# Performance work log

Hardware: AMD Instinct MI355X
Metric: run time of the kernel (lower is better)

The kernel has to match this reference:

```python
import jax, jax.numpy as jnp
import numpy as np

N = 100000
E = 1600000
IN_C = 256
OUT_C = 64


def setup_inputs() -> dict:
    key = jax.random.key(0)
    k1, k2, k3, k4, k5 = jax.random.split(key, 5)
    x = jax.random.normal(k1, (N, IN_C), dtype=jnp.float32)
    edge_index = jax.random.randint(k2, (2, E), 0, N, dtype=jnp.int64)
    edge_weight = jax.random.uniform(k3, (E,), dtype=jnp.float32)
    # GCNConv linear weight (Glorot-style scale) and bias
    W = jax.random.normal(k4, (IN_C, OUT_C), dtype=jnp.float32) * (1.0 / np.sqrt(IN_C))
    b = jax.random.normal(k5, (OUT_C,), dtype=jnp.float32) * 0.01
    return {"x": x, "edge_index": edge_index, "edge_weight": edge_weight, "W": W, "b": b}


def reference(x, edge_index, edge_weight, W, b):
    n = x.shape[0]
    row, col = edge_index[0], edge_index[1]  # source -> target (PyG source_to_target flow)
    # add self-loops with weight 1.0 (GCNConv default add_self_loops=True)
    loop = jnp.arange(n, dtype=edge_index.dtype)
    row = jnp.concatenate([row, loop])
    col = jnp.concatenate([col, loop])
    ew = jnp.concatenate([edge_weight, jnp.ones((n,), dtype=x.dtype)])
    # symmetric normalization: deg computed on target nodes
    deg = jax.ops.segment_sum(ew, col, num_segments=n)
    dinv = jnp.where(deg > 0, jax.lax.rsqrt(deg), 0.0)
    norm = dinv[row] * ew * dinv[col]  # [E+N]
    # dense linear transform first (fewer FLOPs than transforming per-edge)
    h = x @ W  # [N, OUT_C]
    # gather messages from source, scale, scatter-add to target
    out = jax.ops.segment_sum(norm[:, None] * h[row], col, num_segments=n)
    out = out + b
    # activation is None -> module returns (val, ()); we return val
    return out
```

## Files before the change

kernel.cpp:

```cpp
#include <hip/hip_runtime.h>
#include <hip/hip_fp16.h>


#define BS 256
#define EPB2 4096
#define BSH 8
#define CAP 4608

typedef unsigned long long u64;
typedef unsigned int u32;
typedef unsigned short u16;
typedef unsigned char u8;

typedef __attribute__((ext_vector_type(8))) short bf16x8;
typedef __attribute__((ext_vector_type(4))) float f32x4;

__device__ inline u16 f2bf(float f) {
    u32 u = __float_as_uint(f);
    return (u16)((u + 0x7fffu + ((u >> 16) & 1u)) >> 16);
}
__device__ inline u32 pack2bf(float a, float b) {
    return (u32)f2bf(a) | ((u32)f2bf(b) << 16);
}

#define GBM2 128
#define XAP 40

__global__ __launch_bounds__(BS) void k_g4(const float* __restrict__ x,
                                           const float* __restrict__ W,
                                           u16* __restrict__ hh, int n,
                                           const int* __restrict__ row,
                                           const int* __restrict__ col,
                                           const float* __restrict__ ew,
                                           u32* __restrict__ cursor,
                                           u64* __restrict__ pack,
                                           int nbuck, int nblk2, int e) {
    __shared__ __align__(16) u8 smem[24576];
    const int tid = threadIdx.x;
    const int bi = blockIdx.x;
    const bool isScatter = ((bi % 3) == 2) && (bi / 3 < nblk2);

    if (isScatter) {
        u16* bkt  = (u16*)smem;
        u16* sidx = (u16*)(smem + 8192);
        u32* cnt  = (u32*)(smem + 16384);
        u32* scn  = (u32*)(smem + 18432);
        u32* lpos = (u32*)(smem + 20480);
        u32* gb   = (u32*)(smem + 22528);
        int blk = bi / 3;
        int base = blk * EPB2;
        int ej = e - base; if (ej > EPB2) ej = EPB2;

        cnt[tid] = 0; cnt[tid + 256] = 0;
        __syncthreads();
#pragma unroll
        for (int j = 0; j < 16; ++j) {
            int lj = j * BS + tid;
            if (lj < ej) {
                int b = col[base + lj] >> BSH;
                bkt[lj] = (u16)b;
                atomicAdd(&cnt[b], 1u);
            }
        }
        __syncthreads();
        scn[tid] = cnt[tid];
        scn[tid + 256] = cnt[tid + 256];
        __syncthreads();
        for (int off = 1; off < 512; off <<= 1) {
            u32 a0 = (tid >= off) ? scn[tid - off] : 0u;
            u32 a1 = scn[tid + 256 - off];
            __syncthreads();
            scn[tid] += a0;
            scn[tid + 256] += a1;
            __syncthreads();
        }
        for (int t = tid; t < 512; t += 256) {
            u32 c = cnt[t];
            lpos[t] = scn[t] - c;
            if (c) gb[t] = atomicAdd(&cursor[t], c);
        }
        __syncthreads();
#pragma unroll
        for (int j = 0; j < 16; ++j) {
            int lj = j * BS + tid;
            if (lj < ej) {
                u32 p = atomicAdd(&lpos[bkt[lj]], 1u);
                sidx[p] = (u16)lj;
            }
        }
        __syncthreads();
        for (int p = tid; p < ej; p += 256) {
            int lj = sidx[p];
            int b = bkt[lj];
            int i = base + lj;
            __half eh = __float2half(ew[i]);
            u64 en = (u64)(u32)row[i]
                   | ((u64)(u32)(col[i] & 255) << 32)
                   | ((u64)(u16)__half_as_ushort(eh) << 48);
            u32 local = (u32)p - (scn[b] - cnt[b]) + gb[b];
            if (local < CAP) pack[(size_t)b * CAP + local] = en;
        }
        return;
    }
    int sbefore = bi / 3; if (sbefore > nblk2) sbefore = nblk2;
    const int gid = bi - sbefore;
    u16* xa = (u16*)smem;
    u16* wt = (u16*)(smem + 10240);
    const int lane = tid & 63;
    const int wid  = tid >> 6;
    const int lr = lane & 15;
    const int lg = lane >> 4;
    const int rb = gid * GBM2;
    const int wrow = wid * 32;

    f32x4 acc[2][4];
#pragma unroll
    for (int rt = 0; rt < 2; ++rt)
#pragma unroll
        for (int ct = 0; ct < 4; ++ct) acc[rt][ct] = (f32x4){0.f, 0.f, 0.f, 0.f};

    const int srow = tid >> 1;
    const int skh  = (tid & 1) * 16;
    const int wc   = tid >> 2;
    const int wk   = (tid & 3) * 8;

    for (int kc = 0; kc < 256; kc += 32) {
        {
            int gr = rb + srow; if (gr >= n) gr = n - 1;
            const float4* src = reinterpret_cast<const float4*>(&x[(size_t)gr * 256 + kc + skh]);
            float4 a0 = src[0], a1 = src[1], a2 = src[2], a3 = src[3];
            uint4 v0, v1;
            v0.x = pack2bf(a0.x, a0.y); v0.y = pack2bf(a0.z, a0.w);
            v0.z = pack2bf(a1.x, a1.y); v0.w = pack2bf(a1.z, a1.w);
            v1.x = pack2bf(a2.x, a2.y); v1.y = pack2bf(a2.z, a2.w);
            v1.z = pack2bf(a3.x, a3.y); v1.w = pack2bf(a3.z, a3.w);
            *reinterpret_cast<uint4*>(&xa[srow * XAP + skh]) = v0;
            *reinterpret_cast<uint4*>(&xa[srow * XAP + skh + 8]) = v1;
        }
        {
            float w0 = W[(size_t)(kc + wk + 0) * 64 + wc];
            float w1 = W[(size_t)(kc + wk + 1) * 64 + wc];
            float w2 = W[(size_t)(kc + wk + 2) * 64 + wc];
            float w3 = W[(size_t)(kc + wk + 3) * 64 + wc];
            float w4 = W[(size_t)(kc + wk + 4) * 64 + wc];
            float w5 = W[(size_t)(kc + wk + 5) * 64 + wc];
            float w6 = W[(size_t)(kc + wk + 6) * 64 + wc];
            float w7 = W[(size_t)(kc + wk + 7) * 64 + wc];
            u32* dst = reinterpret_cast<u32*>(&wt[wc * XAP + wk]);
            dst[0] = pack2bf(w0, w1);
            dst[1] = pack2bf(w2, w3);
            dst[2] = pack2bf(w4, w5);
            dst[3] = pack2bf(w6, w7);
        }
        __syncthreads();

        bf16x8 af0 = *reinterpret_cast<const bf16x8*>(&xa[(wrow + lr) * XAP + lg * 8]);
        bf16x8 af1 = *reinterpret_cast<const bf16x8*>(&xa[(wrow + 16 + lr) * XAP + lg * 8]);
#pragma unroll
        for (int ct = 0; ct < 4; ++ct) {
            bf16x8 bfr = *reinterpret_cast<const bf16x8*>(&wt[(ct * 16 + lr) * XAP + lg * 8]);
            acc[0][ct] = __builtin_amdgcn_mfma_f32_16x16x32_bf16(af0, bfr, acc[0][ct], 0, 0, 0);
            acc[1][ct] = __builtin_amdgcn_mfma_f32_16x16x32_bf16(af1, bfr, acc[1][ct], 0, 0, 0);
        }
        __syncthreads();
    }

    u16* eo = (u16*)smem;
#pragma unroll
    for (int rt = 0; rt < 2; ++rt) {
#pragma unroll
        for (int reg = 0; reg < 4; ++reg) {
            int r = wrow + rt * 16 + lg * 4 + reg;
#pragma unroll
            for (int ct = 0; ct < 4; ++ct) {
                eo[r * 64 + ct * 16 + lr] =
                    __half_as_ushort(__float2half(acc[rt][ct][reg]));
            }
        }
    }
    __syncthreads();
    {
        const uint4* src = reinterpret_cast<const uint4*>(eo);
        uint4* dst = reinterpret_cast<uint4*>(hh + (size_t)rb * 64);
#pragma unroll
        for (int i = 0; i < 4; ++i) {
            int idx = i * BS + tid;
            if (rb + (idx >> 3) < n) dst[idx] = src[idx];
        }
    }
}

#define MAXB CAP
__global__ __launch_bounds__(512) void k_b2(const u32* __restrict__ cursor,
                                            u64* __restrict__ pack,
                                            float* __restrict__ dinv,
                                            int* __restrict__ offs,
                                            int* __restrict__ ends,
                                            int n, int nbuck) {
    __shared__ u32 lrow[MAXB];
    __shared__ u16 lew[MAXB];
    __shared__ u8  lcl[MAXB];
    __shared__ u32 cnt[256];
    __shared__ float wdeg[256];
    __shared__ u32 pos[256];
    __shared__ float ldsd[256];
    int b = blockIdx.x;
    int tid = threadIdx.x;
    size_t gbase = (size_t)b * CAP;
    int size = (int)cursor[b];
    if (size > MAXB) size = MAXB;
    if (tid < 256) { cnt[tid] = 0; wdeg[tid] = 0.0f; }
    __syncthreads();
    for (int j = tid; j < size; j += 512) {
        u64 en = pack[gbase + j];
        u32 r = (u32)en;
        u32 cl = (u32)(en >> 32) & 255u;
        u16 eh = (u16)(en >> 48);
        lrow[j] = r;
        lcl[j] = (u8)cl;
        lew[j] = eh;
        atomicAdd(&cnt[cl], 1u);
        atomicAdd(&wdeg[cl], __half2float(__ushort_as_half(eh)));
    }
    __syncthreads();
    u32 myc = (tid < 256) ? cnt[tid] : 0;
    for (int off = 1; off < 256; off <<= 1) {
        u32 t = 0;
        if (tid < 256 && tid >= (u32)off) t = cnt[tid - off];
        __syncthreads();
        if (tid < 256) cnt[tid] += t;
        __syncthreads();
    }
    if (tid < 256) {
        u32 st = cnt[tid] - myc;
        pos[tid] = st;
        float dv = rsqrtf(1.0f + wdeg[tid]);
        ldsd[tid] = dv;
        int c = (b << BSH) + tid;
        if (c < n) {
            dinv[c] = dv;
            offs[c] = (int)(gbase + st);
            ends[c] = (int)(gbase + st + myc);
        }
    }
    __syncthreads();
    for (int j = tid; j < size; j += 512) {
        u32 cl = lcl[j];
        u32 r = atomicAdd(&pos[cl], 1u);
        float w = __half2float(__ushort_as_half(lew[j])) * ldsd[cl];
        pack[gbase + r] = ((u64)__float_as_uint(w) << 32) | (u64)lrow[j];
    }
}

__global__ __launch_bounds__(BS) void k_reduce(const u64* __restrict__ sorted,
                                               const int* __restrict__ offs,
                                               const int* __restrict__ ends,
                                               const float* __restrict__ dinv,
                                               const __half2* __restrict__ hh,
                                               const float* __restrict__ bias,
                                               float* __restrict__ out, int n) {
    int node = blockIdx.x * 4 + (threadIdx.x >> 6);
    int lane = threadIdx.x & 63;
    if (node >= n) return;
    int cc  = lane & 31;
    int ehi = lane >> 5;
    int s = offs[node];
    int t = ends[node];
    float ax = 0.0f, ay = 0.0f;
    int j = s;
    for (; j + 7 < t; j += 8) {
        u64 p0 = sorted[j     + ehi];
        u64 p1 = sorted[j + 2 + ehi];
        u64 p2 = sorted[j + 4 + ehi];
        u64 p3 = sorted[j + 6 + ehi];
        int r0 = (int)(u32)p0, r1 = (int)(u32)p1, r2 = (int)(u32)p2, r3 = (int)(u32)p3;
        float n0 = __uint_as_float((u32)(p0 >> 32)) * dinv[r0];
        float n1 = __uint_as_float((u32)(p1 >> 32)) * dinv[r1];
        float n2 = __uint_as_float((u32)(p2 >> 32)) * dinv[r2];
        float n3 = __uint_as_float((u32)(p3 >> 32)) * dinv[r3];
        float2 f0 = __half22float2(hh[(size_t)r0 * 32 + cc]);
        float2 f1 = __half22float2(hh[(size_t)r1 * 32 + cc]);
        float2 f2 = __half22float2(hh[(size_t)r2 * 32 + cc]);
        float2 f3 = __half22float2(hh[(size_t)r3 * 32 + cc]);
        ax += n0 * f0.x; ay += n0 * f0.y;
        ax += n1 * f1.x; ay += n1 * f1.y;
        ax += n2 * f2.x; ay += n2 * f2.y;
        ax += n3 * f3.x; ay += n3 * f3.y;
    }
    for (; j + 1 < t; j += 2) {
        u64 p = sorted[j + ehi];
        int r = (int)(u32)p;
        float nn = __uint_as_float((u32)(p >> 32)) * dinv[r];
        float2 f = __half22float2(hh[(size_t)r * 32 + cc]);
        ax += nn * f.x; ay += nn * f.y;
    }
    if (j < t && ehi == 0) {
        u64 p = sorted[j];
        int r = (int)(u32)p;
        float nn = __uint_as_float((u32)(p >> 32)) * dinv[r];
        float2 f = __half22float2(hh[(size_t)r * 32 + cc]);
        ax += nn * f.x; ay += nn * f.y;
    }
    ax += __shfl_xor(ax, 32);
    ay += __shfl_xor(ay, 32);
    if (ehi == 0) {
        float di = dinv[node];
        float2 fs = __half22float2(hh[(size_t)node * 32 + cc]);
        float2 bb = *reinterpret_cast<const float2*>(&bias[cc * 2]);
        float2 r;
        r.x = ax + di * di * fs.x + bb.x;
        r.y = ay + di * di * fs.y + bb.y;
        reinterpret_cast<float2*>(out)[(size_t)node * 32 + cc] = r;
    }
}

__global__ __launch_bounds__(BS) void k_init_f(float* __restrict__ deg, int n) {
    int i = blockIdx.x * BS + threadIdx.x;
    if (i < n) deg[i] = 1.0f;
}
__global__ __launch_bounds__(BS) void k_count_f(const int* __restrict__ col,
                                                const float* __restrict__ ew,
                                                float* __restrict__ deg, int e) {
    int i = blockIdx.x * BS + threadIdx.x;
    if (i < e) unsafeAtomicAdd(&deg[col[i]], ew[i]);
}
__global__ __launch_bounds__(BS) void k_dinv_f(float* __restrict__ deg, int n) {
    int i = blockIdx.x * BS + threadIdx.x;
    if (i < n) {
        float d = deg[i];
        deg[i] = d > 0.0f ? rsqrtf(d) : 0.0f;
    }
}
__global__ __launch_bounds__(BS) void k_gemm_f(const float* __restrict__ x,
                                               const float* __restrict__ W,
                                               float* __restrict__ h, int n) {
    __shared__ float xsh[4 * 256];
    int b0 = blockIdx.x * 4;
    const float4* xv = reinterpret_cast<const float4*>(x + (size_t)b0 * 256);
    reinterpret_cast<float4*>(xsh)[threadIdx.x] = xv[threadIdx.x];
    __syncthreads();
    int rl = threadIdx.x >> 6;
    int c  = threadIdx.x & 63;
    const float* xr = xsh + rl * 256;
    float acc = 0.0f;
#pragma unroll 8
    for (int k = 0; k < 256; ++k) acc += xr[k] * W[k * 64 + c];
    int r = b0 + rl;
    if (r < n) h[(size_t)r * 64 + c] = acc;
}
__global__ __launch_bounds__(BS) void k_out_init(const float* __restrict__ h,
                                                 const float* __restrict__ dinv,
                                                 const float* __restrict__ bias,
                                                 float* __restrict__ out, int n64) {
    int i = blockIdx.x * BS + threadIdx.x;
    if (i < n64) {
        int r = i >> 6, c = i & 63;
        float di = dinv[r];
        out[i] = bias[c] + di * di * h[i];
    }
}
__global__ __launch_bounds__(BS) void k_scatter(const int* __restrict__ row,
                                                const int* __restrict__ col,
                                                const float* __restrict__ ew,
                                                const float* __restrict__ dinv,
                                                const float* __restrict__ h,
                                                float* __restrict__ out, int e) {
    int idx = blockIdx.x * BS + threadIdx.x;
    int ei = idx >> 6;
    int c  = idx & 63;
    if (ei >= e) return;
    int r = row[ei];
    int t = col[ei];
    float nrm = dinv[r] * ew[ei] * dinv[t];
    unsafeAtomicAdd(&out[(size_t)t * 64 + c], nrm * h[(size_t)r * 64 + c]);
}

extern "C" void kernel_launch(void* const* d_in, const int* in_sizes, int n_in,
                              void* d_out, int out_size, void* d_ws, size_t ws_size,
                              hipStream_t stream) {
    const float* x   = (const float*)d_in[0];
    const int*   ei  = (const int*)d_in[1];
    const float* ew  = (const float*)d_in[2];
    const float* W   = (const float*)d_in[3];
    const float* b   = (const float*)d_in[4];
    float* out = (float*)d_out;

    const int n = in_sizes[0] / 256;
    const int e = in_sizes[1] / 2;
    const int* row = ei;
    const int* col = ei + e;
    const int nbuck = (n + 255) >> 8;
    const int nblk2 = (e + EPB2 - 1) / EPB2;
    const int ngemm = (n + GBM2 - 1) / GBM2;

    size_t off = 0;
    auto alloc = [&](size_t elems) { size_t p = off; off += (elems + 63) & ~63ull; return p; };
    size_t o_cursor = alloc(nbuck);
    size_t o_pack   = alloc((size_t)nbuck * CAP * 2);
    size_t o_offs   = alloc(n);
    size_t o_ends   = alloc(n);
    size_t o_dinv   = alloc(n);
    size_t o_h      = alloc((size_t)n * 32);
    size_t needed = off * 4;

    u32*   wsu = (u32*)d_ws;
    float* wsf = (float*)d_ws;
    int*   wsi = (int*)d_ws;

    if (ws_size >= needed) {
        u32*   cursor = wsu + o_cursor;
        u64*   pack   = (u64*)(wsu + o_pack);
        int*   offs   = wsi + o_offs;
        int*   ends   = wsi + o_ends;
        float* dinv   = wsf + o_dinv;
        u16*   hh     = (u16*)(wsu + o_h);

        hipMemsetAsync(cursor, 0, (size_t)nbuck * 4, stream);
        k_g4<<<ngemm + nblk2, BS, 0, stream>>>(x, W, hh, n,
                                               row, col, ew, cursor, pack,
                                               nbuck, nblk2, e);
        k_b2<<<nbuck, 512, 0, stream>>>(cursor, pack, dinv, offs, ends, n, nbuck);
        k_reduce<<<(n + 3) / 4, BS, 0, stream>>>(pack, offs, ends, dinv,
                                                 (const __half2*)hh, b, out, n);
    } else {
        float* deg = wsf;
        float* h   = wsf + ((n + 63) & ~63);
        const int nb = (n + BS - 1) / BS;
        const int eb = (e + BS - 1) / BS;
        k_init_f<<<nb, BS, 0, stream>>>(deg, n);
        k_count_f<<<eb, BS, 0, stream>>>(col, ew, deg, e);
        k_dinv_f<<<nb, BS, 0, stream>>>(deg, n);
        k_gemm_f<<<(n + 3) / 4, BS, 0, stream>>>(x, W, h, n);
        k_out_init<<<((n * 64) + BS - 1) / BS, BS, 0, stream>>>(h, deg, b, out, n * 64);
        k_scatter<<<((size_t)e * 64 + BS - 1) / BS, BS, 0, stream>>>(row, col, ew, deg, h, out, e);
    }
}
```

Measured before the change: 128.2 us.

## Split degree computation into its own pass and fold source dinv into edge weights

```diff
diff --git a/kernel.cpp b/kernel.cpp
--- a/kernel.cpp
+++ b/kernel.cpp
@@ -190,10 +190,30 @@
     }
 }
 
+__global__ __launch_bounds__(512) void k_dv(const u32* __restrict__ cursor,
+                                            const u64* __restrict__ pack,
+                                            float* __restrict__ dinv, int n) {
+    __shared__ float wdeg[256];
+    int b = blockIdx.x;
+    int tid = threadIdx.x;
+    if (tid < 256) wdeg[tid] = 1.0f;
+    __syncthreads();
+    int size = (int)cursor[b]; if (size > CAP) size = CAP;
+    size_t gbase = (size_t)b * CAP;
+    for (int j = tid; j < size; j += 512) {
+        u64 en = pack[gbase + j];
+        u32 cl = (u32)(en >> 32) & 255u;
+        atomicAdd(&wdeg[cl], __half2float(__ushort_as_half((u16)(en >> 48))));
+    }
+    __syncthreads();
+    int c = (b << BSH) + tid;
+    if (tid < 256 && c < n) dinv[c] = rsqrtf(wdeg[tid]);
+}
+
 #define MAXB CAP
 __global__ __launch_bounds__(512) void k_b2(const u32* __restrict__ cursor,
                                             u64* __restrict__ pack,
-                                            float* __restrict__ dinv,
+                                            const float* __restrict__ dinv,
                                             int* __restrict__ offs,
                                             int* __restrict__ ends,
                                             int n, int nbuck) {
@@ -201,7 +221,6 @@
     __shared__ u16 lew[MAXB];
     __shared__ u8  lcl[MAXB];
     __shared__ u32 cnt[256];
-    __shared__ float wdeg[256];
     __shared__ u32 pos[256];
     __shared__ float ldsd[256];
     int b = blockIdx.x;
@@ -209,18 +228,18 @@
     size_t gbase = (size_t)b * CAP;
     int size = (int)cursor[b];
     if (size > MAXB) size = MAXB;
-    if (tid < 256) { cnt[tid] = 0; wdeg[tid] = 0.0f; }
+    if (tid < 256) {
+        cnt[tid] = 0;
+        int c = (b << BSH) + tid;
+        ldsd[tid] = (c < n) ? dinv[c] : 0.f;
+    }
     __syncthreads();
     for (int j = tid; j < size; j += 512) {
         u64 en = pack[gbase + j];
-        u32 r = (u32)en;
-        u32 cl = (u32)(en >> 32) & 255u;
-        u16 eh = (u16)(en >> 48);
-        lrow[j] = r;
-        lcl[j] = (u8)cl;
-        lew[j] = eh;
-        atomicAdd(&cnt[cl], 1u);
-        atomicAdd(&wdeg[cl], __half2float(__ushort_as_half(eh)));
+        lrow[j] = (u32)en;
+        lcl[j] = (u8)((u32)(en >> 32) & 255u);
+        lew[j] = (u16)(en >> 48);
+        atomicAdd(&cnt[lcl[j]], 1u);
     }
     __syncthreads();
     u32 myc = (tid < 256) ? cnt[tid] : 0;
@@ -234,11 +253,8 @@
     if (tid < 256) {
         u32 st = cnt[tid] - myc;
         pos[tid] = st;
-        float dv = rsqrtf(1.0f + wdeg[tid]);
-        ldsd[tid] = dv;
         int c = (b << BSH) + tid;
         if (c < n) {
-            dinv[c] = dv;
             offs[c] = (int)(gbase + st);
             ends[c] = (int)(gbase + st + myc);
         }
@@ -247,7 +263,7 @@
     for (int j = tid; j < size; j += 512) {
         u32 cl = lcl[j];
         u32 r = atomicAdd(&pos[cl], 1u);
-        float w = __half2float(__ushort_as_half(lew[j])) * ldsd[cl];
+        float w = __half2float(__ushort_as_half(lew[j])) * ldsd[cl] * dinv[lrow[j]];
         pack[gbase + r] = ((u64)__float_as_uint(w) << 32) | (u64)lrow[j];
     }
 }
@@ -274,10 +290,10 @@
         u64 p2 = sorted[j + 4 + ehi];
         u64 p3 = sorted[j + 6 + ehi];
         int r0 = (int)(u32)p0, r1 = (int)(u32)p1, r2 = (int)(u32)p2, r3 = (int)(u32)p3;
-        float n0 = __uint_as_float((u32)(p0 >> 32)) * dinv[r0];
-        float n1 = __uint_as_float((u32)(p1 >> 32)) * dinv[r1];
-        float n2 = __uint_as_float((u32)(p2 >> 32)) * dinv[r2];
-        float n3 = __uint_as_float((u32)(p3 >> 32)) * dinv[r3];
+        float n0 = __uint_as_float((u32)(p0 >> 32));
+        float n1 = __uint_as_float((u32)(p1 >> 32));
+        float n2 = __uint_as_float((u32)(p2 >> 32));
+        float n3 = __uint_as_float((u32)(p3 >> 32));
         float2 f0 = __half22float2(hh[(size_t)r0 * 32 + cc]);
         float2 f1 = __half22float2(hh[(size_t)r1 * 32 + cc]);
         float2 f2 = __half22float2(hh[(size_t)r2 * 32 + cc]);
@@ -290,14 +306,14 @@
     for (; j + 1 < t; j += 2) {
         u64 p = sorted[j + ehi];
         int r = (int)(u32)p;
-        float nn = __uint_as_float((u32)(p >> 32)) * dinv[r];
+        float nn = __uint_as_float((u32)(p >> 32));
         float2 f = __half22float2(hh[(size_t)r * 32 + cc]);
         ax += nn * f.x; ay += nn * f.y;
     }
     if (j < t && ehi == 0) {
         u64 p = sorted[j];
         int r = (int)(u32)p;
-        float nn = __uint_as_float((u32)(p >> 32)) * dinv[r];
+        float nn = __uint_as_float((u32)(p >> 32));
         float2 f = __half22float2(hh[(size_t)r * 32 + cc]);
         ax += nn * f.x; ay += nn * f.y;
     }
@@ -419,6 +435,7 @@
         k_g4<<<ngemm + nblk2, BS, 0, stream>>>(x, W, hh, n,
                                                row, col, ew, cursor, pack,
                                                nbuck, nblk2, e);
+        k_dv<<<nbuck, 512, 0, stream>>>(cursor, pack, dinv, n);
         k_b2<<<nbuck, 512, 0, stream>>>(cursor, pack, dinv, offs, ends, n, nbuck);
         k_reduce<<<(n + 3) / 4, BS, 0, stream>>>(pack, offs, ends, dinv,
                                                  (const __half2*)hh, b, out, n);
```

New measurement: 135.2 us. 1.05x slower.

## Replace global bucket cursors with per-block counts and deterministic two-level gather

Applied to the files above, without the earlier changes.

```diff
diff --git a/kernel.cpp b/kernel.cpp
--- a/kernel.cpp
+++ b/kernel.cpp
@@ -6,6 +6,7 @@
 #define EPB2 4096
 #define BSH 8
 #define CAP 4608
+#define NBK 512
 
 typedef unsigned long long u64;
 typedef unsigned int u32;
@@ -32,7 +33,8 @@
                                            const int* __restrict__ row,
                                            const int* __restrict__ col,
                                            const float* __restrict__ ew,
-                                           u32* __restrict__ cursor,
+                                           u16* __restrict__ cntg,
+                                           u16* __restrict__ scng,
                                            u64* __restrict__ pack,
                                            int nbuck, int nblk2, int e) {
     __shared__ __align__(16) u8 smem[24576];
@@ -46,7 +48,6 @@
         u32* cnt  = (u32*)(smem + 16384);
         u32* scn  = (u32*)(smem + 18432);
         u32* lpos = (u32*)(smem + 20480);
-        u32* gb   = (u32*)(smem + 22528);
         int blk = bi / 3;
         int base = blk * EPB2;
         int ej = e - base; if (ej > EPB2) ej = EPB2;
@@ -76,8 +77,10 @@
         }
         for (int t = tid; t < 512; t += 256) {
             u32 c = cnt[t];
-            lpos[t] = scn[t] - c;
-            if (c) gb[t] = atomicAdd(&cursor[t], c);
+            u32 st = scn[t] - c;
+            lpos[t] = st;
+            cntg[(size_t)blk * NBK + t] = (u16)c;
+            scng[(size_t)blk * NBK + t] = (u16)st;
         }
         __syncthreads();
 #pragma unroll
@@ -91,14 +94,12 @@
         __syncthreads();
         for (int p = tid; p < ej; p += 256) {
             int lj = sidx[p];
-            int b = bkt[lj];
             int i = base + lj;
             __half eh = __float2half(ew[i]);
             u64 en = (u64)(u32)row[i]
                    | ((u64)(u32)(col[i] & 255) << 32)
                    | ((u64)(u16)__half_as_ushort(eh) << 48);
-            u32 local = (u32)p - (scn[b] - cnt[b]) + gb[b];
-            if (local < CAP) pack[(size_t)b * CAP + local] = en;
+            pack[(size_t)blk * EPB2 + p] = en;
         }
         return;
     }
@@ -191,12 +192,14 @@
 }
 
 #define MAXB CAP
-__global__ __launch_bounds__(512) void k_b2(const u32* __restrict__ cursor,
-                                            u64* __restrict__ pack,
+__global__ __launch_bounds__(512) void k_b2(const u16* __restrict__ cntg,
+                                            const u16* __restrict__ scng,
+                                            const u64* __restrict__ pack,
+                                            u64* __restrict__ pack2,
                                             float* __restrict__ dinv,
                                             int* __restrict__ offs,
                                             int* __restrict__ ends,
-                                            int n, int nbuck) {
+                                            int n, int nblk) {
     __shared__ u32 lrow[MAXB];
     __shared__ u16 lew[MAXB];
     __shared__ u8  lcl[MAXB];
@@ -204,23 +207,38 @@
     __shared__ float wdeg[256];
     __shared__ u32 pos[256];
     __shared__ float ldsd[256];
+    __shared__ u32 s[512];
     int b = blockIdx.x;
     int tid = threadIdx.x;
-    size_t gbase = (size_t)b * CAP;
-    int size = (int)cursor[b];
-    if (size > MAXB) size = MAXB;
+
     if (tid < 256) { cnt[tid] = 0; wdeg[tid] = 0.0f; }
+    u32 myLen = 0, myStart = 0;
+    if (tid < nblk) {
+        myLen   = cntg[(size_t)tid * NBK + b];
+        myStart = (u32)tid * EPB2 + scng[(size_t)tid * NBK + b];
+    }
+    s[tid] = myLen;
     __syncthreads();
-    for (int j = tid; j < size; j += 512) {
-        u64 en = pack[gbase + j];
-        u32 r = (u32)en;
-        u32 cl = (u32)(en >> 32) & 255u;
-        u16 eh = (u16)(en >> 48);
-        lrow[j] = r;
-        lcl[j] = (u8)cl;
-        lew[j] = eh;
-        atomicAdd(&cnt[cl], 1u);
-        atomicAdd(&wdeg[cl], __half2float(__ushort_as_half(eh)));
+    for (int off = 1; off < 512; off <<= 1) {
+        u32 t = (tid >= off) ? s[tid - off] : 0u;
+        __syncthreads();
+        s[tid] += t;
+        __syncthreads();
+    }
+    u32 base = s[tid] - myLen;
+    int size = (int)s[511]; if (size > MAXB) size = MAXB;
+    for (u32 k = 0; k < myLen; ++k) {
+        u32 idx = base + k;
+        if (idx < (u32)MAXB) {
+            u64 en = pack[myStart + k];
+            u32 cl = (u32)(en >> 32) & 255u;
+            u16 eh = (u16)(en >> 48);
+            lrow[idx] = (u32)en;
+            lcl[idx] = (u8)cl;
+            lew[idx] = eh;
+            atomicAdd(&cnt[cl], 1u);
+            atomicAdd(&wdeg[cl], __half2float(__ushort_as_half(eh)));
+        }
     }
     __syncthreads();
     u32 myc = (tid < 256) ? cnt[tid] : 0;
@@ -231,6 +249,7 @@
         if (tid < 256) cnt[tid] += t;
         __syncthreads();
     }
+    size_t gbase = (size_t)b * CAP;
     if (tid < 256) {
         u32 st = cnt[tid] - myc;
         pos[tid] = st;
@@ -248,7 +267,7 @@
         u32 cl = lcl[j];
         u32 r = atomicAdd(&pos[cl], 1u);
         float w = __half2float(__ushort_as_half(lew[j])) * ldsd[cl];
-        pack[gbase + r] = ((u64)__float_as_uint(w) << 32) | (u64)lrow[j];
+        pack2[gbase + r] = ((u64)__float_as_uint(w) << 32) | (u64)lrow[j];
     }
 }
 
@@ -395,12 +414,14 @@
 
     size_t off = 0;
     auto alloc = [&](size_t elems) { size_t p = off; off += (elems + 63) & ~63ull; return p; };
-    size_t o_cursor = alloc(nbuck);
-    size_t o_pack   = alloc((size_t)nbuck * CAP * 2);
-    size_t o_offs   = alloc(n);
-    size_t o_ends   = alloc(n);
-    size_t o_dinv   = alloc(n);
-    size_t o_h      = alloc((size_t)n * 32);
+    size_t o_cntg  = alloc(((size_t)nblk2 * NBK + 1) / 2);
+    size_t o_scng  = alloc(((size_t)nblk2 * NBK + 1) / 2);
+    size_t o_pack  = alloc((size_t)nblk2 * EPB2 * 2);
+    size_t o_pack2 = alloc((size_t)nbuck * CAP * 2);
+    size_t o_offs  = alloc(n);
+    size_t o_ends  = alloc(n);
+    size_t o_dinv  = alloc(n);
+    size_t o_h     = alloc((size_t)n * 32);
     size_t needed = off * 4;
 
     u32*   wsu = (u32*)d_ws;
@@ -408,19 +429,21 @@
     int*   wsi = (int*)d_ws;
 
     if (ws_size >= needed) {
-        u32*   cursor = wsu + o_cursor;
-        u64*   pack   = (u64*)(wsu + o_pack);
-        int*   offs   = wsi + o_offs;
-        int*   ends   = wsi + o_ends;
-        float* dinv   = wsf + o_dinv;
-        u16*   hh     = (u16*)(wsu + o_h);
-
-        hipMemsetAsync(cursor, 0, (size_t)nbuck * 4, stream);
+        u16*   cntg  = (u16*)(wsu + o_cntg);
+        u16*   scng  = (u16*)(wsu + o_scng);
+        u64*   pack  = (u64*)(wsu + o_pack);
+        u64*   pack2 = (u64*)(wsu + o_pack2);
+        int*   offs  = wsi + o_offs;
+        int*   ends  = wsi + o_ends;
+        float* dinv  = wsf + o_dinv;
+        u16*   hh    = (u16*)(wsu + o_h);
+
         k_g4<<<ngemm + nblk2, BS, 0, stream>>>(x, W, hh, n,
-                                               row, col, ew, cursor, pack,
+                                               row, col, ew, cntg, scng, pack,
                                                nbuck, nblk2, e);
-        k_b2<<<nbuck, 512, 0, stream>>>(cursor, pack, dinv, offs, ends, n, nbuck);
-        k_reduce<<<(n + 3) / 4, BS, 0, stream>>>(pack, offs, ends, dinv,
+        k_b2<<<nbuck, 512, 0, stream>>>(cntg, scng, pack, pack2,
+                                        dinv, offs, ends, n, nblk2);
+        k_reduce<<<(n + 3) / 4, BS, 0, stream>>>(pack2, offs, ends, dinv,
                                                  (const __half2*)hh, b, out, n);
     } else {
         float* deg = wsf;
```

Result: faster. 123.5 us (median of 2 runs) (-3.6%).
